# Kernel tuning notes

Hardware: AMD Instinct MI355X
Metric: run time of the kernel (lower is better)

Reference implementation:

```python
import jax, jax.numpy as jnp
import numpy as np

D_MODEL = 1024
NUM_HEADS = 16
HEAD_DIM = D_MODEL // NUM_HEADS
B, S, S_CACHE = 2, 2048, 2048


def setup_inputs() -> dict:
    key = jax.random.key(0)
    ks = jax.random.split(key, 7)
    scale = 1.0 / np.sqrt(D_MODEL)
    return {
        "x": jax.random.normal(ks[0], (B, S, D_MODEL), dtype=jnp.float32),
        "kv_k": jax.random.normal(ks[1], (B, NUM_HEADS, S_CACHE, HEAD_DIM), dtype=jnp.float32),
        "kv_v": jax.random.normal(ks[2], (B, NUM_HEADS, S_CACHE, HEAD_DIM), dtype=jnp.float32),
        "W_Q": jax.random.normal(ks[3], (D_MODEL, D_MODEL), dtype=jnp.float32) * scale,
        "W_K": jax.random.normal(ks[4], (D_MODEL, D_MODEL), dtype=jnp.float32) * scale,
        "W_V": jax.random.normal(ks[5], (D_MODEL, D_MODEL), dtype=jnp.float32) * scale,
        "W_O": jax.random.normal(ks[6], (D_MODEL, D_MODEL), dtype=jnp.float32) * scale,
    }


def reference(x, kv_k, kv_v, W_Q, W_K, W_V, W_O):
    b, s, d = x.shape
    h, hd = NUM_HEADS, HEAD_DIM
    # projections: [B,S,D] -> [B,H,S,hd]
    def proj(W):
        return jnp.einsum('bsd,de->bse', x, W).reshape(b, s, h, hd).transpose(0, 2, 1, 3)
    Q = proj(W_Q)
    K = proj(W_K)
    V = proj(W_V)
    # KV-cache concat along sequence axis
    K = jnp.concatenate([kv_k, K], axis=2)  # [B,H,S_tot,hd]
    V = jnp.concatenate([kv_v, V], axis=2)
    scores = jnp.einsum('bhqd,bhkd->bhqk', Q, K) / jnp.sqrt(jnp.float32(hd))
    attn = jax.nn.softmax(scores, axis=-1)
    out = jnp.einsum('bhqk,bhkd->bhqd', attn, V)  # [B,H,S,hd]
    out = out.transpose(0, 2, 1, 3).reshape(b, s, d)
    out = jnp.einsum('bsd,de->bse', out, W_O)
    return (out, (K, V))
```

## Files before the change

kernel.cpp:

```cpp
#include <hip/hip_runtime.h>
#include <hip/hip_bf16.h>

typedef unsigned int u32;
typedef unsigned short u16;
typedef __bf16 bf16x8 __attribute__((ext_vector_type(8)));
typedef float f32x4 __attribute__((ext_vector_type(4)));

typedef const __attribute__((address_space(1))) u32 gas_u32;
typedef __attribute__((address_space(3))) u32 las_u32;

#define ST 4096

__device__ __forceinline__ u16 f2bf(float f) {
    u32 u = __builtin_bit_cast(u32, f);
    u32 r = (u + 0x7FFFu + ((u >> 16) & 1u)) >> 16;
    return (u16)r;
}

__device__ __forceinline__ u32 cvtpk(float lo, float hi) {
    u32 r;
    asm("v_cvt_pk_bf16_f32 %0, %1, %2" : "=v"(r) : "v"(lo), "v"(hi));
    return r;
}

__device__ __forceinline__ uint4 pack8(float4 a, float4 b) {
    uint4 o;
    u16* e = (u16*)&o;
    e[0] = f2bf(a.x); e[1] = f2bf(a.y); e[2] = f2bf(a.z); e[3] = f2bf(a.w);
    e[4] = f2bf(b.x); e[5] = f2bf(b.y); e[6] = f2bf(b.z); e[7] = f2bf(b.w);
    return o;
}

__device__ __forceinline__ void gload_lds16(const u16* g, u16* l) {
    __builtin_amdgcn_global_load_lds((gas_u32*)g, (las_u32*)l, 16, 0, 0);
}

__global__ __launch_bounds__(256) void k_prep(const float* __restrict__ x, u16* __restrict__ xb,
                                              const float* w0, const float* w1,
                                              const float* w2, const float* w3, u16* wt,
                                              const float* __restrict__ k_in,
                                              const float* __restrict__ v_in,
                                              float* kc, float* vc, u16* kb, u16* vbT) {
    __shared__ u16 tile[64 * 72];
    const int bid = blockIdx.x;
    const int t = threadIdx.x;

    if (bid < 2048) {
        int i = bid * 256 + t;
        const float4* s = (const float4*)(x + i * 8);
        *(uint4*)(xb + i * 8) = pack8(s[0], s[1]);
        return;
    }

    const int r = t >> 3, c8 = (t & 7) * 8;
    if (bid < 3072) {
        int idx = bid - 2048;
        int z = idx >> 8, rem = idx & 255;
        int tc = (rem & 15) * 64, tr = (rem >> 4) * 64;
        const float* W = (z == 0) ? w0 : (z == 1) ? w1 : (z == 2) ? w2 : w3;
        u16* WT = wt + z * (1024 * 1024);
#pragma unroll
        for (int p = 0; p < 2; ++p) {
            int rr = r + p * 32;
            const float4* src = (const float4*)&W[(tr + rr) * 1024 + tc + c8];
            *(uint4*)&tile[rr * 72 + c8] = pack8(src[0], src[1]);
        }
        __syncthreads();
#pragma unroll
        for (int p = 0; p < 2; ++p) {
            int rr = r + p * 32;
            uint4 vv;
            u16* e = (u16*)&vv;
#pragma unroll
            for (int j = 0; j < 8; ++j) e[j] = tile[(c8 + j) * 72 + rr];
            *(uint4*)&WT[(tc + rr) * 1024 + tr + c8] = vv;
        }
        return;
    }

    {
        int idx = bid - 3072;
        int kt = idx & 31, bh = idx >> 5;
#pragma unroll
        for (int p = 0; p < 2; ++p) {
            int rr = r + p * 32;
            int srow = (bh * 2048 + kt * 64 + rr) * 64 + c8;
            int drow = (bh * 4096 + kt * 64 + rr) * 64 + c8;
            const float4* ks = (const float4*)&k_in[srow];
            const float4* vs = (const float4*)&v_in[srow];
            float4 k0 = ks[0], k1 = ks[1], v0 = vs[0], v1 = vs[1];
            *(float4*)&kc[drow] = k0; *(float4*)&kc[drow + 4] = k1;
            *(float4*)&vc[drow] = v0; *(float4*)&vc[drow + 4] = v1;
            *(uint4*)&kb[drow] = pack8(k0, k1);
            *(uint4*)&tile[rr * 72 + c8] = pack8(v0, v1);
        }
        __syncthreads();
#pragma unroll
        for (int p = 0; p < 2; ++p) {
            int dd = r + p * 32;
            uint4 vv;
            u16* e = (u16*)&vv;
#pragma unroll
            for (int j = 0; j < 8; ++j) e[j] = tile[(c8 + j) * 72 + dd];
            *(uint4*)&vbT[(bh * 64 + dd) * 4096 + kt * 64 + c8] = vv;
        }
    }
}

__global__ __launch_bounds__(256) void k_cvt_x(const float* __restrict__ x, u16* __restrict__ xb) {
    int t = blockIdx.x * 256 + threadIdx.x;
    const float4* s = (const float4*)(x + t * 8);
    *(uint4*)(xb + t * 8) = pack8(s[0], s[1]);
}

__global__ __launch_bounds__(256) void k_transpose(const float* w0, const float* w1,
                                                   const float* w2, const float* w3, u16* wt) {
    int z = blockIdx.z;
    const float* W = (z == 0) ? w0 : (z == 1) ? w1 : (z == 2) ? w2 : w3;
    u16* WT = wt + z * (1024 * 1024);
    __shared__ u16 tile[64 * 72];
    int t = threadIdx.x;
    int tr = blockIdx.y * 64, tc = blockIdx.x * 64;
#pragma unroll
    for (int p = 0; p < 2; ++p) {
        int r = (t >> 3) + p * 32, c8 = (t & 7) * 8;
        const float4* src = (const float4*)&W[(tr + r) * 1024 + tc + c8];
        *(uint4*)&tile[r * 72 + c8] = pack8(src[0], src[1]);
    }
    __syncthreads();
#pragma unroll
    for (int p = 0; p < 2; ++p) {
        int r = (t >> 3) + p * 32, c8 = (t & 7) * 8;
        uint4 vv;
        u16* e = (u16*)&vv;
#pragma unroll
        for (int j = 0; j < 8; ++j) e[j] = tile[(c8 + j) * 72 + r];
        *(uint4*)&WT[(tc + r) * 1024 + tr + c8] = vv;
    }
}

__global__ __launch_bounds__(256) void k_copy_cache(const float4* __restrict__ k_in,
                                                    const float4* __restrict__ v_in,
                                                    float4* k_out, float4* v_out) {
    int t = blockIdx.x * 256 + threadIdx.x;
    int bh = t >> 15;
    int i = t & 32767;
    k_out[bh * 65536 + i] = k_in[t];
    v_out[bh * 65536 + i] = v_in[t];
}

__device__ __forceinline__ void gemm_loop(const u16* A, const u16* BT, int mrow, int ncol,
                                          u16* lds_a, u16* lds_b, f32x4 (&acc)[4][4]) {
    const int t = threadIdx.x;
    const int lane = t & 63;
    const int w = t >> 6;
    const int wm = (w >> 1) * 64, wn = (w & 1) * 64;
    const int l15 = lane & 15, lg = lane >> 4;

    const u16* gA = A + (mrow + (t >> 2)) * 1024 + (t & 3) * 8;
    const u16* gB = BT + (ncol + (t >> 2)) * 1024 + (t & 3) * 8;
    u16* la = lds_a + t * 8;
    u16* lb = lds_b + t * 8;

    for (int k0 = 0; k0 < 1024; k0 += 32) {
        gload_lds16(gA + k0, la);
        gload_lds16(gA + k0 + 64 * 1024, la + 64 * 32);
        gload_lds16(gB + k0, lb);
        gload_lds16(gB + k0 + 64 * 1024, lb + 64 * 32);
        __syncthreads();
        bf16x8 af[4], bfr[4];
#pragma unroll
        for (int m = 0; m < 4; ++m)
            af[m] = *(const bf16x8*)&lds_a[(wm + m * 16 + l15) * 32 + lg * 8];
#pragma unroll
        for (int n = 0; n < 4; ++n)
            bfr[n] = *(const bf16x8*)&lds_b[(wn + n * 16 + l15) * 32 + lg * 8];
#pragma unroll
        for (int m = 0; m < 4; ++m)
#pragma unroll
            for (int n = 0; n < 4; ++n)
                acc[m][n] = __builtin_amdgcn_mfma_f32_16x16x32_bf16(af[m], bfr[n], acc[m][n], 0, 0, 0);
        __syncthreads();
    }
}

__global__ __launch_bounds__(256) void k_gemm_qkv(const u16* X, const u16* WT,
                                                  u16* qb, float* kc, float* vc,
                                                  u16* kb, u16* vbT) {
    __shared__ u16 smem[128 * 136];
    const int z = blockIdx.z;
    const int mrow = blockIdx.x * 128, ncol = blockIdx.y * 128;

    f32x4 acc[4][4];
#pragma unroll
    for (int m = 0; m < 4; ++m)
#pragma unroll
        for (int n = 0; n < 4; ++n) acc[m][n] = (f32x4){0.f, 0.f, 0.f, 0.f};

    gemm_loop(X, WT + z * (1024 * 1024), mrow, ncol, smem, smem + 8192, acc);

    const int t = threadIdx.x, lane = t & 63, w = t >> 6;
    const int wm = (w >> 1) * 64, wn = (w & 1) * 64;
    const int l15 = lane & 15, lg = lane >> 4;
#pragma unroll
    for (int m = 0; m < 4; ++m)
#pragma unroll
        for (int n = 0; n < 4; ++n)
#pragma unroll
            for (int r = 0; r < 4; ++r) {
                int gr = mrow + wm + m * 16 + lg * 4 + r;
                int gc = ncol + wn + n * 16 + l15;
                int b = gr >> 11, s = gr & 2047, h = gc >> 6, d = gc & 63;
                if (z == 0) {
                    qb[((b * 16 + h) * 2048 + s) * 64 + d] = f2bf(acc[m][n][r]);
                } else {
                    int idx = ((b * 16 + h) * 4096 + 2048 + s) * 64 + d;
                    if (z == 1) { kc[idx] = acc[m][n][r]; if (kb) kb[idx] = f2bf(acc[m][n][r]); }
                    else         vc[idx] = acc[m][n][r];
                }
            }

    if (z == 2 && vbT) {
#pragma unroll
        for (int m = 0; m < 4; ++m)
#pragma unroll
            for (int n = 0; n < 4; ++n)
#pragma unroll
                for (int r = 0; r < 4; ++r)
                    smem[(wn + n * 16 + l15) * 136 + wm + m * 16 + lg * 4 + r] =
                        f2bf(acc[m][n][r]);
        __syncthreads();
        const int c = t >> 1, half = t & 1;
        const int gc = ncol + c, h2 = gc >> 6, d2 = gc & 63;
        const int bb = mrow >> 11, sbase = mrow & 2047;
        u16* dst = vbT + (size_t)((bb * 16 + h2) * 64 + d2) * 4096 + 2048 + sbase + half * 64;
        const u16* srcp = &smem[c * 136 + half * 64];
#pragma unroll
        for (int j = 0; j < 8; ++j)
            ((uint4*)dst)[j] = *(const uint4*)&srcp[j * 8];
    }
}

__global__ __launch_bounds__(256) void k_gemm_o(const u16* A, const u16* WT, float* out) {
    __shared__ u16 lds_a[128 * 32];
    __shared__ u16 lds_b[128 * 32];
    const int mrow = blockIdx.x * 128, ncol = blockIdx.y * 128;

    f32x4 acc[4][4];
#pragma unroll
    for (int m = 0; m < 4; ++m)
#pragma unroll
        for (int n = 0; n < 4; ++n) acc[m][n] = (f32x4){0.f, 0.f, 0.f, 0.f};

    gemm_loop(A, WT, mrow, ncol, lds_a, lds_b, acc);

    const int t = threadIdx.x, lane = t & 63, w = t >> 6;
    const int wm = (w >> 1) * 64, wn = (w & 1) * 64;
    const int l15 = lane & 15, lg = lane >> 4;
#pragma unroll
    for (int m = 0; m < 4; ++m)
#pragma unroll
        for (int n = 0; n < 4; ++n)
#pragma unroll
            for (int r = 0; r < 4; ++r) {
                int gr = mrow + wm + m * 16 + lg * 4 + r;
                int gc = ncol + wn + n * 16 + l15;
                out[gr * 1024 + gc] = acc[m][n][r];
            }
}

#define LOG2E_SCALE 0.18033688f
#define RESCALE_THR 11.0f
__global__ __launch_bounds__(512) void k_attn_c(const u16* __restrict__ qb,
                                                const u16* __restrict__ kb,
                                                const u16* __restrict__ vbT,
                                                u16* __restrict__ aws) {
    __shared__ u16 lk[2][4096];
    __shared__ u16 lv[2][4096];
    __shared__ u16 lp[8][16 * 72];

    const int t = threadIdx.x, lane = t & 63, w = t >> 6;
    const int l15 = lane & 15, lg = lane >> 4;
    const int n = blockIdx.x;
    const int wg = (n & 7) * 64 + (n >> 3);
    const int qt = wg & 15, bh = wg >> 4;
    const int b = bh >> 4, h = bh & 15;

    const u16* Qb  = qb + (bh * 2048 + qt * 128 + w * 16) * 64;
    const u16* Kbh = kb + bh * (ST * 64);
    const u16* VbT = vbT + bh * (64 * ST);

    const int kr = t >> 3, kc8 = t & 7;
    const int swz8 = (kc8 ^ (kr & 7)) * 8;
    const int srcK = kr * 64 + swz8;
    const int srcV = kr * ST + swz8;

    bf16x8 qf[2];
#pragma unroll
    for (int ds = 0; ds < 2; ++ds)
        qf[ds] = *(const bf16x8*)&Qb[l15 * 64 + ds * 32 + lg * 8];

    f32x4 o[4];
    float m_ = -INFINITY, ls = 0.f;
#pragma unroll
    for (int i = 0; i < 4; ++i) o[i] = (f32x4){0.f, 0.f, 0.f, 0.f};

    gload_lds16(Kbh + srcK, &lk[0][t * 8]);
    gload_lds16(VbT + srcV, &lv[0][t * 8]);
    __syncthreads();

#define TILE_BODY(CUR, NXT, KT)                                                             \
    {                                                                                       \
        const bool more = ((KT) + 1 < ST / 64);                                             \
        if (more) {                                                                         \
            gload_lds16(Kbh + ((KT) + 1) * 4096 + srcK, &lk[NXT][t * 8]);                   \
            gload_lds16(VbT + ((KT) + 1) * 64 + srcV, &lv[NXT][t * 8]);                     \
        }                                                                                   \
        f32x4 s[4];                                                                         \
        __builtin_amdgcn_s_setprio(1);                                                      \
        _Pragma("unroll")                                                                   \
        for (int ni = 0; ni < 4; ++ni) {                                                    \
            f32x4 a = (f32x4){0.f, 0.f, 0.f, 0.f};                                          \
            _Pragma("unroll")                                                               \
            for (int ds = 0; ds < 2; ++ds) {                                                \
                bf16x8 kf = *(const bf16x8*)&lk[CUR][(ni * 16 + l15) * 64 +                 \
                                                    (((ds * 4 + lg) ^ (l15 & 7)) * 8)];     \
                a = __builtin_amdgcn_mfma_f32_16x16x32_bf16(kf, qf[ds], a, 0, 0, 0);        \
            }                                                                               \
            s[ni] = a * LOG2E_SCALE;                                                        \
        }                                                                                   \
        __builtin_amdgcn_s_setprio(0);                                                      \
        float t0 = fmaxf(fmaxf(s[0][0], s[0][1]), fmaxf(s[0][2], s[0][3]));                 \
        float t1 = fmaxf(fmaxf(s[1][0], s[1][1]), fmaxf(s[1][2], s[1][3]));                 \
        float t2 = fmaxf(fmaxf(s[2][0], s[2][1]), fmaxf(s[2][2], s[2][3]));                 \
        float t3 = fmaxf(fmaxf(s[3][0], s[3][1]), fmaxf(s[3][2], s[3][3]));                 \
        float tm = fmaxf(fmaxf(t0, t1), fmaxf(t2, t3));                                     \
        if (__any(tm > m_ + RESCALE_THR)) {                                                 \
            tm = fmaxf(tm, __shfl_xor(tm, 16));                                             \
            tm = fmaxf(tm, __shfl_xor(tm, 32));                                             \
            float mn = fmaxf(m_, tm);                                                       \
            float corr = exp2f(m_ - mn);                                                    \
            ls *= corr;                                                                     \
            m_ = mn;                                                                        \
            _Pragma("unroll")                                                               \
            for (int r = 0; r < 4; ++r) {                                                   \
                float cr = __shfl(corr, lg * 4 + r);                                        \
                _Pragma("unroll")                                                           \
                for (int dt = 0; dt < 4; ++dt) o[dt][r] *= cr;                              \
            }                                                                               \
        }                                                                                   \
        _Pragma("unroll")                                                                   \
        for (int ni = 0; ni < 4; ++ni) {                                                    \
            float p0 = exp2f(s[ni][0] - m_);                                                \
            float p1 = exp2f(s[ni][1] - m_);                                                \
            float p2 = exp2f(s[ni][2] - m_);                                                \
            float p3 = exp2f(s[ni][3] - m_);                                                \
            ls += (p0 + p1) + (p2 + p3);                                                    \
            *(uint2*)&lp[w][l15 * 72 + ni * 16 + lg * 4] =                                  \
                make_uint2(cvtpk(p0, p1), cvtpk(p2, p3));                                   \
        }                                                                                   \
        bf16x8 pf[2];                                                                       \
        _Pragma("unroll")                                                                   \
        for (int kss = 0; kss < 2; ++kss)                                                   \
            pf[kss] = *(const bf16x8*)&lp[w][l15 * 72 + kss * 32 + lg * 8];                 \
        __builtin_amdgcn_s_setprio(1);                                                      \
        _Pragma("unroll")                                                                   \
        for (int dt = 0; dt < 4; ++dt) {                                                    \
            const int dd = dt * 16 + l15;                                                   \
            _Pragma("unroll")                                                               \
            for (int kss = 0; kss < 2; ++kss) {                                             \
                bf16x8 vf = *(const bf16x8*)&lv[CUR][dd * 64 +                              \
                                                    (((kss * 4 + lg) ^ (dd & 7)) * 8)];     \
                o[dt] = __builtin_amdgcn_mfma_f32_16x16x32_bf16(pf[kss], vf, o[dt], 0, 0, 0);\
            }                                                                               \
        }                                                                                   \
        __builtin_amdgcn_s_setprio(0);                                                      \
        __syncthreads();                                                                    \
    }

    for (int kt = 0; kt < ST / 64; kt += 2) {
        TILE_BODY(0, 1, kt)
        TILE_BODY(1, 0, kt + 1)
    }
#undef TILE_BODY

    ls += __shfl_xor(ls, 16);
    ls += __shfl_xor(ls, 32);
    const int qrow = qt * 128 + w * 16 + lg * 4;
#pragma unroll
    for (int r = 0; r < 4; ++r) {
        float lr = __shfl(ls, lg * 4 + r);
        float inv = 1.f / lr;
#pragma unroll
        for (int dt = 0; dt < 4; ++dt) {
            int sg = qrow + r;
            int col = h * 64 + dt * 16 + l15;
            aws[(b * 2048 + sg) * 1024 + col] = f2bf(o[dt][r] * inv);
        }
    }
}

__global__ __launch_bounds__(256) void k_attn(const u16* qb, const float* kc,
                                              const float* vc, u16* aws) {
    __shared__ u16 lk[64 * 72];
    __shared__ u16 lvt[64 * 72];
    __shared__ u16 lp[4][16 * 72];

    const int t = threadIdx.x, lane = t & 63, w = t >> 6;
    const int l15 = lane & 15, lg = lane >> 4;
    const int qt = blockIdx.x;
    const int bh = blockIdx.y;
    const int b = bh >> 4, h = bh & 15;

    const u16* Qb = qb + (bh * 2048 + qt * 64 + w * 16) * 64;
    const float* Kb = kc + bh * (ST * 64);
    const float* Vb = vc + bh * (ST * 64);

    bf16x8 qf[2];
#pragma unroll
    for (int ds = 0; ds < 2; ++ds)
        qf[ds] = *(const bf16x8*)&Qb[l15 * 64 + ds * 32 + lg * 8];

    f32x4 o[4];
    float m_[4], ls[4];
#pragma unroll
    for (int i = 0; i < 4; ++i) { o[i] = (f32x4){0.f, 0.f, 0.f, 0.f}; m_[i] = -INFINITY; ls[i] = 0.f; }

    for (int kt = 0; kt < ST / 64; ++kt) {
        const float* ks = Kb + kt * 64 * 64;
        const float* vs = Vb + kt * 64 * 64;
#pragma unroll
        for (int p = 0; p < 2; ++p) {
            int r = (t >> 3) + p * 32, c8 = (t & 7) * 8;
            const float4* k4 = (const float4*)&ks[r * 64 + c8];
            *(uint4*)&lk[r * 72 + c8] = pack8(k4[0], k4[1]);
            const float4* v4 = (const float4*)&vs[r * 64 + c8];
            uint4 vv = pack8(v4[0], v4[1]);
            const u16* e = (const u16*)&vv;
#pragma unroll
            for (int j = 0; j < 8; ++j) lvt[(c8 + j) * 72 + r] = e[j];
        }
        __syncthreads();

        f32x4 s[4];
#pragma unroll
        for (int ni = 0; ni < 4; ++ni) {
            f32x4 a = (f32x4){0.f, 0.f, 0.f, 0.f};
#pragma unroll
            for (int ds = 0; ds < 2; ++ds) {
                bf16x8 kf = *(const bf16x8*)&lk[(ni * 16 + l15) * 72 + ds * 32 + lg * 8];
                a = __builtin_amdgcn_mfma_f32_16x16x32_bf16(qf[ds], kf, a, 0, 0, 0);
            }
            s[ni] = a * 0.125f;
        }

#pragma unroll
        for (int r = 0; r < 4; ++r) {
            float tm = fmaxf(fmaxf(s[0][r], s[1][r]), fmaxf(s[2][r], s[3][r]));
#pragma unroll
            for (int off = 1; off < 16; off <<= 1) tm = fmaxf(tm, __shfl_xor(tm, off));
            float mn = fmaxf(m_[r], tm);
            float corr = __expf(m_[r] - mn);
            float rs = 0.f;
#pragma unroll
            for (int ni = 0; ni < 4; ++ni) {
                float p = __expf(s[ni][r] - mn);
                s[ni][r] = p;
                rs += p;
            }
#pragma unroll
            for (int off = 1; off < 16; off <<= 1) rs += __shfl_xor(rs, off);
            ls[r] = ls[r] * corr + rs;
            m_[r] = mn;
#pragma unroll
            for (int dt = 0; dt < 4; ++dt) o[dt][r] *= corr;
        }

#pragma unroll
        for (int ni = 0; ni < 4; ++ni)
#pragma unroll
            for (int r = 0; r < 4; ++r)
                lp[w][(lg * 4 + r) * 72 + ni * 16 + l15] = f2bf(s[ni][r]);

#pragma unroll
        for (int dt = 0; dt < 4; ++dt) {
#pragma unroll
            for (int kss = 0; kss < 2; ++kss) {
                bf16x8 pf = *(const bf16x8*)&lp[w][l15 * 72 + kss * 32 + lg * 8];
                bf16x8 vf = *(const bf16x8*)&lvt[(dt * 16 + l15) * 72 + kss * 32 + lg * 8];
                o[dt] = __builtin_amdgcn_mfma_f32_16x16x32_bf16(pf, vf, o[dt], 0, 0, 0);
            }
        }
        __syncthreads();
    }

    const int qrow = qt * 64 + w * 16 + lg * 4;
#pragma unroll
    for (int r = 0; r < 4; ++r) {
        float inv = 1.f / ls[r];
#pragma unroll
        for (int dt = 0; dt < 4; ++dt) {
            int sg = qrow + r;
            int col = h * 64 + dt * 16 + l15;
            aws[(b * 2048 + sg) * 1024 + col] = f2bf(o[dt][r] * inv);
        }
    }
}

extern "C" void kernel_launch(void* const* d_in, const int* in_sizes, int n_in,
                              void* d_out, int out_size, void* d_ws, size_t ws_size,
                              hipStream_t stream) {
    const float* x   = (const float*)d_in[0];
    const float* kvk = (const float*)d_in[1];
    const float* kvv = (const float*)d_in[2];
    const float* wq  = (const float*)d_in[3];
    const float* wk  = (const float*)d_in[4];
    const float* wv  = (const float*)d_in[5];
    const float* wo  = (const float*)d_in[6];

    float* out = (float*)d_out;
    float* kc  = out + 4194304;
    float* vc  = kc + 8388608;

    u16* qb = (u16*)d_out;
    u16* xb = (u16*)d_out + 4194304;

    if (ws_size >= (size_t)50331648) {
        u16* wt  = (u16*)d_ws;
        u16* kb  = wt + 4194304;
        u16* vbT = kb + 8388608;
        u16* aws = vbT + 8388608;

        k_prep<<<dim3(4096), dim3(256), 0, stream>>>(x, xb, wq, wk, wv, wo, wt,
                                                     kvk, kvv, kc, vc, kb, vbT);
        k_gemm_qkv<<<dim3(32, 8, 3), dim3(256), 0, stream>>>(xb, wt, qb, kc, vc, kb, vbT);
        k_attn_c<<<dim3(512), dim3(512), 0, stream>>>(qb, kb, vbT, aws);
        k_gemm_o<<<dim3(32, 8), dim3(256), 0, stream>>>(aws, wt + 3 * 1048576, out);
    } else {
        u16* wt  = (u16*)d_ws;
        u16* xb2 = wt + 4 * 1048576;
        u16* aws = xb2;

        k_cvt_x<<<dim3(2048), dim3(256), 0, stream>>>(x, xb2);
        k_transpose<<<dim3(16, 16, 4), dim3(256), 0, stream>>>(wq, wk, wv, wo, wt);
        k_copy_cache<<<dim3(4096), dim3(256), 0, stream>>>((const float4*)kvk, (const float4*)kvv,
                                                           (float4*)kc, (float4*)vc);
        k_gemm_qkv<<<dim3(32, 8, 3), dim3(256), 0, stream>>>(xb2, wt, qb, kc, vc, nullptr, nullptr);
        k_attn<<<dim3(32, 32), dim3(256), 0, stream>>>(qb, kc, vc, aws);
        k_gemm_o<<<dim3(32, 8), dim3(256), 0, stream>>>(aws, wt + 3 * 1048576, out);
    }
}
```

Measured before the change: 228.4 us.

## Split attention KV range in two halves and merge partials in a combine kernel

The cached-attention kernel now splits the 4096-key range into two halves, launching twice as many workgroups, each covering half the keys for a 128-query tile. Each half writes a normalized bf16 partial output plus its per-row max and sum to scratch buffers that reuse already-consumed workspace regions. A new elementwise kernel merges the two partials with log-sum-exp weights before the output projection. The aim is more parallelism and better CU occupancy and load balance. The cost is an extra launch, extra memory traffic for the partials, and some added rounding from storing partials in bf16.

```diff
diff --git a/kernel.cpp b/kernel.cpp
--- a/kernel.cpp
+++ b/kernel.cpp
@@ -15,6 +15,10 @@
     u32 u = __builtin_bit_cast(u32, f);
     u32 r = (u + 0x7FFFu + ((u >> 16) & 1u)) >> 16;
     return (u16)r;
+}
+__device__ __forceinline__ float bf2f(u16 b) {
+    u32 u = ((u32)b) << 16;
+    return __builtin_bit_cast(float, u);
 }
 
 __device__ __forceinline__ u32 cvtpk(float lo, float hi) {
@@ -271,10 +275,12 @@
 
 #define LOG2E_SCALE 0.18033688f
 #define RESCALE_THR 11.0f
-__global__ __launch_bounds__(512) void k_attn_c(const u16* __restrict__ qb,
+__global__ __launch_bounds__(512) void k_attn_s(const u16* __restrict__ qb,
                                                 const u16* __restrict__ kb,
                                                 const u16* __restrict__ vbT,
-                                                u16* __restrict__ aws) {
+                                                u16* __restrict__ p0,
+                                                u16* __restrict__ p1,
+                                                float2* __restrict__ mls) {
     __shared__ u16 lk[2][4096];
     __shared__ u16 lv[2][4096];
     __shared__ u16 lp[8][16 * 72];
@@ -282,13 +288,15 @@
     const int t = threadIdx.x, lane = t & 63, w = t >> 6;
     const int l15 = lane & 15, lg = lane >> 4;
     const int n = blockIdx.x;
-    const int wg = (n & 7) * 64 + (n >> 3);
-    const int qt = wg & 15, bh = wg >> 4;
+    const int wg = (n & 7) * 128 + (n >> 3);
+    const int half = wg >> 9;
+    const int rest = wg & 511;
+    const int qt = rest & 15, bh = rest >> 4;
     const int b = bh >> 4, h = bh & 15;
 
     const u16* Qb  = qb + (bh * 2048 + qt * 128 + w * 16) * 64;
-    const u16* Kbh = kb + bh * (ST * 64);
-    const u16* VbT = vbT + bh * (64 * ST);
+    const u16* Kb2 = kb + bh * (ST * 64) + half * 32 * 4096;
+    const u16* Vb2 = vbT + bh * (64 * ST) + half * 32 * 64;
 
     const int kr = t >> 3, kc8 = t & 7;
     const int swz8 = (kc8 ^ (kr & 7)) * 8;
@@ -305,16 +313,16 @@
 #pragma unroll
     for (int i = 0; i < 4; ++i) o[i] = (f32x4){0.f, 0.f, 0.f, 0.f};
 
-    gload_lds16(Kbh + srcK, &lk[0][t * 8]);
-    gload_lds16(VbT + srcV, &lv[0][t * 8]);
+    gload_lds16(Kb2 + srcK, &lk[0][t * 8]);
+    gload_lds16(Vb2 + srcV, &lv[0][t * 8]);
     __syncthreads();
 
 #define TILE_BODY(CUR, NXT, KT)                                                             \
     {                                                                                       \
-        const bool more = ((KT) + 1 < ST / 64);                                             \
+        const bool more = ((KT) + 1 < 32);                                                  \
         if (more) {                                                                         \
-            gload_lds16(Kbh + ((KT) + 1) * 4096 + srcK, &lk[NXT][t * 8]);                   \
-            gload_lds16(VbT + ((KT) + 1) * 64 + srcV, &lv[NXT][t * 8]);                     \
+            gload_lds16(Kb2 + ((KT) + 1) * 4096 + srcK, &lk[NXT][t * 8]);                   \
+            gload_lds16(Vb2 + ((KT) + 1) * 64 + srcV, &lv[NXT][t * 8]);                     \
         }                                                                                   \
         f32x4 s[4];                                                                         \
         __builtin_amdgcn_s_setprio(1);                                                      \
@@ -351,13 +359,13 @@
         }                                                                                   \
         _Pragma("unroll")                                                                   \
         for (int ni = 0; ni < 4; ++ni) {                                                    \
-            float p0 = exp2f(s[ni][0] - m_);                                                \
-            float p1 = exp2f(s[ni][1] - m_);                                                \
-            float p2 = exp2f(s[ni][2] - m_);                                                \
-            float p3 = exp2f(s[ni][3] - m_);                                                \
-            ls += (p0 + p1) + (p2 + p3);                                                    \
+            float p0_ = exp2f(s[ni][0] - m_);                                               \
+            float p1_ = exp2f(s[ni][1] - m_);                                               \
+            float p2_ = exp2f(s[ni][2] - m_);                                               \
+            float p3_ = exp2f(s[ni][3] - m_);                                               \
+            ls += (p0_ + p1_) + (p2_ + p3_);                                                \
             *(uint2*)&lp[w][l15 * 72 + ni * 16 + lg * 4] =                                  \
-                make_uint2(cvtpk(p0, p1), cvtpk(p2, p3));                                   \
+                make_uint2(cvtpk(p0_, p1_), cvtpk(p2_, p3_));                               \
         }                                                                                   \
         bf16x8 pf[2];                                                                       \
         _Pragma("unroll")                                                                   \
@@ -378,7 +386,7 @@
         __syncthreads();                                                                    \
     }
 
-    for (int kt = 0; kt < ST / 64; kt += 2) {
+    for (int kt = 0; kt < 32; kt += 2) {
         TILE_BODY(0, 1, kt)
         TILE_BODY(1, 0, kt + 1)
     }
@@ -386,6 +394,7 @@
 
     ls += __shfl_xor(ls, 16);
     ls += __shfl_xor(ls, 32);
+    u16* po = half ? p1 : p0;
     const int qrow = qt * 128 + w * 16 + lg * 4;
 #pragma unroll
     for (int r = 0; r < 4; ++r) {
@@ -395,9 +404,38 @@
         for (int dt = 0; dt < 4; ++dt) {
             int sg = qrow + r;
             int col = h * 64 + dt * 16 + l15;
-            aws[(b * 2048 + sg) * 1024 + col] = f2bf(o[dt][r] * inv);
-        }
-    }
+            po[(b * 2048 + sg) * 1024 + col] = f2bf(o[dt][r] * inv);
+        }
+    }
+    if (lane < 16)
+        mls[half * 65536 + ((b * 16 + h) << 11) + qt * 128 + w * 16 + lane] =
+            make_float2(m_, ls);
+}
+
+__global__ __launch_bounds__(256) void k_comb(const u16* __restrict__ p0,
+                                              u16* __restrict__ p1,
+                                              const float2* __restrict__ mls) {
+    int i = (blockIdx.x * 256 + threadIdx.x) * 8;
+    int row = i >> 10;
+    int b = row >> 11, s = row & 2047;
+    int h = (i & 1023) >> 6;
+    int mi = ((b * 16 + h) << 11) + s;
+    float2 a0 = mls[mi], a1 = mls[65536 + mi];
+    float M = fmaxf(a0.x, a1.x);
+    float w0 = a0.y * exp2f(a0.x - M);
+    float w1 = a1.y * exp2f(a1.x - M);
+    float inv = 1.f / (w0 + w1);
+    w0 *= inv; w1 *= inv;
+    uint4 u0 = *(const uint4*)&p0[i];
+    uint4 u1 = *(const uint4*)&p1[i];
+    const u16* e0 = (const u16*)&u0;
+    const u16* e1 = (const u16*)&u1;
+    uint4 ou;
+    u16* eo = (u16*)&ou;
+#pragma unroll
+    for (int j = 0; j < 8; ++j)
+        eo[j] = f2bf(w0 * bf2f(e0[j]) + w1 * bf2f(e1[j]));
+    *(uint4*)&p1[i] = ou;
 }
 
 __global__ __launch_bounds__(256) void k_attn(const u16* qb, const float* kc,
@@ -531,11 +569,16 @@
         u16* vbT = kb + 8388608;
         u16* aws = vbT + 8388608;
 
+        u16* p0 = xb;
+        u16* p1 = aws;
+        float2* mls = (float2*)wt;
+
         k_prep<<<dim3(4096), dim3(256), 0, stream>>>(x, xb, wq, wk, wv, wo, wt,
                                                      kvk, kvv, kc, vc, kb, vbT);
         k_gemm_qkv<<<dim3(32, 8, 3), dim3(256), 0, stream>>>(xb, wt, qb, kc, vc, kb, vbT);
-        k_attn_c<<<dim3(512), dim3(512), 0, stream>>>(qb, kb, vbT, aws);
-        k_gemm_o<<<dim3(32, 8), dim3(256), 0, stream>>>(aws, wt + 3 * 1048576, out);
+        k_attn_s<<<dim3(1024), dim3(512), 0, stream>>>(qb, kb, vbT, p0, p1, mls);
+        k_comb<<<dim3(2048), dim3(256), 0, stream>>>(p0, p1, mls);
+        k_gemm_o<<<dim3(32, 8), dim3(256), 0, stream>>>(p1, wt + 3 * 1048576, out);
     } else {
         u16* wt  = (u16*)d_ws;
         u16* xb2 = wt + 4 * 1048576;
```

Result: slower. 234.7 us (+2.8%).
